# Kernel optimization log

Hardware: AMD Instinct MI355X
Metric: run time of the kernel (lower is better)

The kernel has to match this reference:

```python
import jax, jax.numpy as jnp
import numpy as np

IN_DIM = 64
OUT_DIM = 64


def setup_inputs() -> dict:
    key = jax.random.key(0)
    k1, k2, k3, k4, k5, k6 = jax.random.split(key, 6)
    N, E = 50000, 800000
    features = jax.random.normal(k1, (N, IN_DIM), dtype=jnp.float32)
    src_idx = jax.random.randint(k2, (E,), 0, N, dtype=jnp.int64)
    # torch nn.Linear-style init (uniform +/- 1/sqrt(fan_in)); stored as [in, out]
    s1 = 1.0 / np.sqrt(IN_DIM)
    s2 = 1.0 / np.sqrt(OUT_DIM)
    W1 = jax.random.uniform(k3, (IN_DIM, OUT_DIM), jnp.float32, -s1, s1)
    b1 = jax.random.uniform(k4, (OUT_DIM,), jnp.float32, -s1, s1)
    W2 = jax.random.uniform(k5, (OUT_DIM, OUT_DIM), jnp.float32, -s2, s2)
    b2 = jax.random.uniform(k6, (OUT_DIM,), jnp.float32, -s2, s2)
    return {"features": features, "src_idx": src_idx, "W1": W1, "b1": b1, "W2": W2, "b2": b2}


def reference(features, src_idx, W1, b1, W2, b2):
    # gather source-node features per edge: [E, in_dim]
    x = features[src_idx]
    # Linear -> ReLU -> Linear -> ReLU
    h = jax.nn.relu(x @ W1 + b1)
    out = jax.nn.relu(h @ W2 + b2)  # [E, out_dim] == 'feature_n'
    return out
```

## Files before the change

### kernel.cpp

```cpp
#include <hip/hip_runtime.h>

typedef float f32x4 __attribute__((ext_vector_type(4)));
typedef _Float16 f16;
typedef f16 f16x8 __attribute__((ext_vector_type(8)));


__global__ __launch_bounds__(256) void cvt_kernel(
    const f32x4* __restrict__ in, f16x8* __restrict__ outv, int n8)
{
    const int stride = gridDim.x * blockDim.x;
    for (int i = blockIdx.x * blockDim.x + threadIdx.x; i < n8; i += stride) {
        const f32x4 a = in[2 * i];
        const f32x4 b = in[2 * i + 1];
        f16x8 o;
        #pragma unroll
        for (int j = 0; j < 4; ++j) { o[j] = (f16)a[j]; o[4 + j] = (f16)b[j]; }
        outv[i] = o;
    }
}

__global__ __launch_bounds__(256) void fused_mlp_kernel(
    const f16* __restrict__ feat16,
    const int* __restrict__ src,
    const float* __restrict__ W1, const float* __restrict__ b1,
    const float* __restrict__ W2, const float* __restrict__ b2,
    float* __restrict__ out, int E, int ntiles)
{
    __shared__ f16 hl[4][16][72];

    const int lane = threadIdx.x & 63;
    const int wv   = threadIdx.x >> 6;
    const int l15  = lane & 15;
    const int q    = lane >> 4;

    const int gw = blockIdx.x * 4 + wv;
    const int nw = gridDim.x * 4;

    f16x8 B1f[4][2], B2f[4][2];
    #pragma unroll
    for (int t = 0; t < 4; ++t) {
        #pragma unroll
        for (int s = 0; s < 2; ++s) {
            f16x8 r1, r2;
            #pragma unroll
            for (int j = 0; j < 8; ++j) {
                const int kk = s * 32 + q * 8 + j;
                r1[j] = (f16)W1[kk * 64 + t * 16 + l15];
                r2[j] = (f16)W2[kk * 64 + t * 16 + l15];
            }
            B1f[t][s] = r1;
            B2f[t][s] = r2;
        }
    }
    float bb1[4], bb2[4];
    #pragma unroll
    for (int t = 0; t < 4; ++t) {
        bb1[t] = b1[t * 16 + l15];
        bb2[t] = b2[t * 16 + l15];
    }

    for (int tile = gw; tile < ntiles; tile += nw) {
        const int e0 = tile * 16;
        int er = e0 + l15;
        if (er >= E) er = E - 1;
        const int n = src[er];

        const f16* fp = feat16 + (long long)n * 64;
        const f16x8 A0 = *(const f16x8*)(fp + q * 8);
        const f16x8 A1 = *(const f16x8*)(fp + 32 + q * 8);

        f32x4 acc[4];
        #pragma unroll
        for (int t = 0; t < 4; ++t) acc[t] = (f32x4){bb1[t], bb1[t], bb1[t], bb1[t]};
        #pragma unroll
        for (int t = 0; t < 4; ++t) {
            acc[t] = __builtin_amdgcn_mfma_f32_16x16x32_f16(A0, B1f[t][0], acc[t], 0, 0, 0);
            acc[t] = __builtin_amdgcn_mfma_f32_16x16x32_f16(A1, B1f[t][1], acc[t], 0, 0, 0);
        }

        #pragma unroll
        for (int t = 0; t < 4; ++t)
            #pragma unroll
            for (int i = 0; i < 4; ++i)
                hl[wv][q * 4 + i][t * 16 + l15] = (f16)fmaxf(acc[t][i], 0.0f);

        const f16x8 A2a = *(const f16x8*)&hl[wv][l15][q * 8];
        const f16x8 A2b = *(const f16x8*)&hl[wv][l15][32 + q * 8];

        f32x4 acc2[4];
        #pragma unroll
        for (int t = 0; t < 4; ++t) acc2[t] = (f32x4){bb2[t], bb2[t], bb2[t], bb2[t]};
        #pragma unroll
        for (int t = 0; t < 4; ++t) {
            acc2[t] = __builtin_amdgcn_mfma_f32_16x16x32_f16(A2a, B2f[t][0], acc2[t], 0, 0, 0);
            acc2[t] = __builtin_amdgcn_mfma_f32_16x16x32_f16(A2b, B2f[t][1], acc2[t], 0, 0, 0);
        }

        #pragma unroll
        for (int t = 0; t < 4; ++t)
            #pragma unroll
            for (int i = 0; i < 4; ++i) {
                const int row = e0 + q * 4 + i;
                if (row < E)
                    out[(long long)row * 64 + t * 16 + l15] = fmaxf(acc2[t][i], 0.0f);
            }
    }
}

__device__ __forceinline__ float bcast(float v, int l) {
    return __int_as_float(__builtin_amdgcn_readlane(__float_as_int(v), l));
}

__global__ __launch_bounds__(256, 3) void mlp_nodes_kernel(
    const float* __restrict__ features,
    const int* __restrict__ idx,
    const float* __restrict__ W1, const float* __restrict__ b1,
    const float* __restrict__ W2, const float* __restrict__ b2,
    float* __restrict__ out, int nrows)
{
    const int lane   = threadIdx.x & 63;
    const int wid    = (blockIdx.x * blockDim.x + threadIdx.x) >> 6;
    const int nwaves = (gridDim.x * blockDim.x) >> 6;

    float w1c[64], w2c[64];
    #pragma unroll
    for (int k = 0; k < 64; ++k) w1c[k] = W1[k * 64 + lane];
    #pragma unroll
    for (int k = 0; k < 64; ++k) w2c[k] = W2[k * 64 + lane];
    const float hb = b1[lane];
    const float yb = b2[lane];

    for (int row = wid; row < nrows; row += nwaves) {
        const int n = idx ? idx[row] : row;
        const float x = features[(long long)n * 64 + lane];
        float a0 = hb, a1 = 0.f, a2 = 0.f, a3 = 0.f;
        #pragma unroll
        for (int k = 0; k < 64; k += 4) {
            a0 = fmaf(bcast(x, k + 0), w1c[k + 0], a0);
            a1 = fmaf(bcast(x, k + 1), w1c[k + 1], a1);
            a2 = fmaf(bcast(x, k + 2), w1c[k + 2], a2);
            a3 = fmaf(bcast(x, k + 3), w1c[k + 3], a3);
        }
        const float h = fmaxf((a0 + a1) + (a2 + a3), 0.0f);
        float c0 = yb, c1 = 0.f, c2 = 0.f, c3 = 0.f;
        #pragma unroll
        for (int k = 0; k < 64; k += 4) {
            c0 = fmaf(bcast(h, k + 0), w2c[k + 0], c0);
            c1 = fmaf(bcast(h, k + 1), w2c[k + 1], c1);
            c2 = fmaf(bcast(h, k + 2), w2c[k + 2], c2);
            c3 = fmaf(bcast(h, k + 3), w2c[k + 3], c3);
        }
        out[(long long)row * 64 + lane] = fmaxf((c0 + c1) + (c2 + c3), 0.0f);
    }
}

extern "C" void kernel_launch(void* const* d_in, const int* in_sizes, int n_in,
                              void* d_out, int out_size, void* d_ws, size_t ws_size,
                              hipStream_t stream) {
    const float* features = (const float*)d_in[0];
    const int*   src      = (const int*)  d_in[1];
    const float* W1       = (const float*)d_in[2];
    const float* b1       = (const float*)d_in[3];
    const float* W2       = (const float*)d_in[4];
    const float* b2       = (const float*)d_in[5];
    float* out = (float*)d_out;

    const int N = in_sizes[0] / 64;
    const int E = in_sizes[1];

    const size_t need = (size_t)N * 64 * sizeof(f16);
    if (ws_size >= need) {
        f16* feat16 = (f16*)d_ws;
        cvt_kernel<<<1024, 256, 0, stream>>>(
            (const f32x4*)features, (f16x8*)feat16, N * 8);
        const int ntiles = (E + 15) / 16;
        fused_mlp_kernel<<<1024, 256, 0, stream>>>(
            feat16, src, W1, b1, W2, b2, out, E, ntiles);
    } else {
        mlp_nodes_kernel<<<3072, 256, 0, stream>>>(
            features, src, W1, b1, W2, b2, out, E);
    }
}
```

Baseline: 67.18 us.

## Prefetch next tile's gathered features and vectorize output stores via LDS

Software-pipelines the gather so each wave issues the index and feature loads for its next tile before running the MFMAs on the current one, hiding gather latency behind compute. It also stages the second-layer results through a padded shared-memory buffer, so full tiles are written as 16-byte vector stores instead of scattered 4-byte stores. In exchange it uses more registers and about 17 KB of extra LDS per block, which may lower occupancy. A leftover no-op scope block remains in the code.

```diff
diff --git a/kernel.cpp b/kernel.cpp
--- a/kernel.cpp
+++ b/kernel.cpp
@@ -26,7 +26,8 @@
     const float* __restrict__ W2, const float* __restrict__ b2,
     float* __restrict__ out, int E, int ntiles)
 {
-    __shared__ f16 hl[4][16][72];
+    __shared__ f16  hl[4][16][72];
+    __shared__ float ol[4][16][68];
 
     const int lane = threadIdx.x & 63;
     const int wv   = threadIdx.x >> 6;
@@ -59,15 +60,32 @@
         bb2[t] = b2[t * 16 + l15];
     }
 
-    for (int tile = gw; tile < ntiles; tile += nw) {
+    int tile = gw;
+    if (tile >= ntiles) return;
+
+    {
+        int er = tile * 16 + l15;
+        if (er >= E) er = E - 1;
+    }
+    int er0 = tile * 16 + l15; if (er0 >= E) er0 = E - 1;
+    int n = src[er0];
+    const f16* fp0 = feat16 + (long long)n * 64;
+    f16x8 A0 = *(const f16x8*)(fp0 + q * 8);
+    f16x8 A1 = *(const f16x8*)(fp0 + 32 + q * 8);
+
+    while (tile < ntiles) {
         const int e0 = tile * 16;
-        int er = e0 + l15;
-        if (er >= E) er = E - 1;
-        const int n = src[er];
-
-        const f16* fp = feat16 + (long long)n * 64;
-        const f16x8 A0 = *(const f16x8*)(fp + q * 8);
-        const f16x8 A1 = *(const f16x8*)(fp + 32 + q * 8);
+        const int tile_n = tile + nw;
+
+        f16x8 nA0, nA1;
+        if (tile_n < ntiles) {
+            int er = tile_n * 16 + l15;
+            if (er >= E) er = E - 1;
+            const int nn = src[er];
+            const f16* fp = feat16 + (long long)nn * 64;
+            nA0 = *(const f16x8*)(fp + q * 8);
+            nA1 = *(const f16x8*)(fp + 32 + q * 8);
+        }
 
         f32x4 acc[4];
         #pragma unroll
@@ -96,14 +114,31 @@
             acc2[t] = __builtin_amdgcn_mfma_f32_16x16x32_f16(A2b, B2f[t][1], acc2[t], 0, 0, 0);
         }
 
-        #pragma unroll
-        for (int t = 0; t < 4; ++t)
-            #pragma unroll
-            for (int i = 0; i < 4; ++i) {
-                const int row = e0 + q * 4 + i;
-                if (row < E)
-                    out[(long long)row * 64 + t * 16 + l15] = fmaxf(acc2[t][i], 0.0f);
+        if (e0 + 16 <= E) {
+            #pragma unroll
+            for (int t = 0; t < 4; ++t)
+                #pragma unroll
+                for (int i = 0; i < 4; ++i)
+                    ol[wv][q * 4 + i][t * 16 + l15] = fmaxf(acc2[t][i], 0.0f);
+            #pragma unroll
+            for (int j = 0; j < 4; ++j) {
+                const f32x4 v = *(const f32x4*)&ol[wv][4 * j + q][l15 * 4];
+                *(f32x4*)&out[(long long)(e0 + 4 * j + q) * 64 + l15 * 4] = v;
             }
+        } else {
+            #pragma unroll
+            for (int t = 0; t < 4; ++t)
+                #pragma unroll
+                for (int i = 0; i < 4; ++i) {
+                    const int row = e0 + q * 4 + i;
+                    if (row < E)
+                        out[(long long)row * 64 + t * 16 + l15] = fmaxf(acc2[t][i], 0.0f);
+                }
+        }
+
+        A0 = nA0;
+        A1 = nA1;
+        tile = tile_n;
     }
 }
 
```

Measured after the change: 66.10 us. Within noise of the previous version (-1.6%).

## Compute MLP per node once and scatter results to edges via bucketed slots

Applied to the files above, without the earlier changes.

Rather than running the MLP on each of the 800k gathered edge rows, the kernel first buckets edge ids by source node using atomic counters into fixed-capacity slots (with an overflow list). It then runs the MLP once per node (50k rows) and scatters each node's output row to all its edges with vectorized stores. This removes most of the redundant matmul work and the separate fp16 conversion pass. In exchange it adds a memset, an atomic bucketing pass, scattered writes, and a capped overflow buffer that could drop edges for highly skewed inputs.

```diff
diff --git a/kernel.cpp b/kernel.cpp
--- a/kernel.cpp
+++ b/kernel.cpp
@@ -4,29 +4,42 @@
 typedef _Float16 f16;
 typedef f16 f16x8 __attribute__((ext_vector_type(8)));
 
-
-__global__ __launch_bounds__(256) void cvt_kernel(
-    const f32x4* __restrict__ in, f16x8* __restrict__ outv, int n8)
+#define MAXDEG 56
+#define OVF_CAP 4096
+
+
+__global__ __launch_bounds__(256) void fill_slots_kernel(
+    const int* __restrict__ src, unsigned* __restrict__ cnt,
+    unsigned* __restrict__ slots, unsigned* __restrict__ ovf,
+    unsigned* __restrict__ ovfc, int E)
 {
     const int stride = gridDim.x * blockDim.x;
-    for (int i = blockIdx.x * blockDim.x + threadIdx.x; i < n8; i += stride) {
-        const f32x4 a = in[2 * i];
-        const f32x4 b = in[2 * i + 1];
-        f16x8 o;
-        #pragma unroll
-        for (int j = 0; j < 4; ++j) { o[j] = (f16)a[j]; o[4 + j] = (f16)b[j]; }
-        outv[i] = o;
-    }
-}
-
-__global__ __launch_bounds__(256) void fused_mlp_kernel(
-    const f16* __restrict__ feat16,
+    for (int e = blockIdx.x * blockDim.x + threadIdx.x; e < E; e += stride) {
+        const int n = src[e];
+        const unsigned slot = atomicAdd(&cnt[n], 1u);
+        if (slot < MAXDEG) {
+            slots[(long long)n * MAXDEG + slot] = (unsigned)e;
+        } else {
+            const unsigned o = atomicAdd(ovfc, 1u);
+            if (o < OVF_CAP) ovf[o] = (unsigned)e;
+        }
+    }
+}
+
+__global__ __launch_bounds__(256) void bcast_kernel(
+    const float* __restrict__ feat,
     const int* __restrict__ src,
     const float* __restrict__ W1, const float* __restrict__ b1,
     const float* __restrict__ W2, const float* __restrict__ b2,
-    float* __restrict__ out, int E, int ntiles)
+    const unsigned* __restrict__ cnt,
+    const unsigned* __restrict__ slots,
+    const unsigned* __restrict__ ovf,
+    const unsigned* __restrict__ ovfc,
+    float* __restrict__ out, int N, int E)
 {
-    __shared__ f16 hl[4][16][72];
+    __shared__ f16   hl[4][16][72];
+    __shared__ float ol[4][16][68];
+    __shared__ int   se[4][16];
 
     const int lane = threadIdx.x & 63;
     const int wv   = threadIdx.x >> 6;
@@ -59,15 +72,24 @@
         bb2[t] = b2[t * 16 + l15];
     }
 
-    for (int tile = gw; tile < ntiles; tile += nw) {
-        const int e0 = tile * 16;
-        int er = e0 + l15;
-        if (er >= E) er = E - 1;
-        const int n = src[er];
-
-        const f16* fp = feat16 + (long long)n * 64;
-        const f16x8 A0 = *(const f16x8*)(fp + q * 8);
-        const f16x8 A1 = *(const f16x8*)(fp + 32 + q * 8);
+    const int ntile = (N + 15) >> 4;
+    for (int tile = gw; tile < ntile; tile += nw) {
+        const int r0 = tile << 4;
+        const int rr = (r0 + l15 < N) ? (r0 + l15) : (N - 1);
+        const float* p = feat + (long long)rr * 64;
+
+        f16x8 A0, A1;
+        {
+            const f32x4 u0 = *(const f32x4*)(p + q * 8);
+            const f32x4 u1 = *(const f32x4*)(p + q * 8 + 4);
+            const f32x4 u2 = *(const f32x4*)(p + 32 + q * 8);
+            const f32x4 u3 = *(const f32x4*)(p + 32 + q * 8 + 4);
+            #pragma unroll
+            for (int j = 0; j < 4; ++j) {
+                A0[j] = (f16)u0[j]; A0[4 + j] = (f16)u1[j];
+                A1[j] = (f16)u2[j]; A1[4 + j] = (f16)u3[j];
+            }
+        }
 
         f32x4 acc[4];
         #pragma unroll
@@ -77,7 +99,6 @@
             acc[t] = __builtin_amdgcn_mfma_f32_16x16x32_f16(A0, B1f[t][0], acc[t], 0, 0, 0);
             acc[t] = __builtin_amdgcn_mfma_f32_16x16x32_f16(A1, B1f[t][1], acc[t], 0, 0, 0);
         }
-
         #pragma unroll
         for (int t = 0; t < 4; ++t)
             #pragma unroll
@@ -99,15 +120,95 @@
         #pragma unroll
         for (int t = 0; t < 4; ++t)
             #pragma unroll
-            for (int i = 0; i < 4; ++i) {
-                const int row = e0 + q * 4 + i;
-                if (row < E)
-                    out[(long long)row * 64 + t * 16 + l15] = fmaxf(acc2[t][i], 0.0f);
-            }
-    }
-}
-
-__device__ __forceinline__ float bcast(float v, int l) {
+            for (int i = 0; i < 4; ++i)
+                ol[wv][q * 4 + i][t * 16 + l15] = fmaxf(acc2[t][i], 0.0f);
+
+        int dv = 0;
+        if (r0 + l15 < N) {
+            unsigned c = cnt[r0 + l15];
+            dv = (int)(c < MAXDEG ? c : MAXDEG);
+        }
+
+        #pragma unroll
+        for (int r = 0; r < 16; ++r) {
+            const int deg = __builtin_amdgcn_readlane(dv, r);
+            if (deg == 0) continue;
+            const unsigned* sl = slots + (long long)(r0 + r) * MAXDEG;
+            const f32x4 v = *(const f32x4*)&ol[wv][r][l15 * 4];
+            for (int base = 0; base < deg; base += 4) {
+                const int k = base + q;
+                if (k < deg) {
+                    const int eid = (int)sl[k];
+                    *(f32x4*)&out[(long long)eid * 64 + l15 * 4] = v;
+                }
+            }
+        }
+    }
+
+    const int novf_raw = (int)ovfc[0];
+    const int novf = novf_raw < OVF_CAP ? novf_raw : OVF_CAP;
+    const int nt2 = (novf + 15) >> 4;
+    for (int t2 = gw; t2 < nt2; t2 += nw) {
+        const int i0 = t2 << 4;
+        const int ii = (i0 + l15 < novf) ? (i0 + l15) : (novf - 1);
+        const int e = (int)ovf[ii];
+        const int n = src[e];
+        const float* p = feat + (long long)n * 64;
+
+        f16x8 A0, A1;
+        {
+            const f32x4 u0 = *(const f32x4*)(p + q * 8);
+            const f32x4 u1 = *(const f32x4*)(p + q * 8 + 4);
+            const f32x4 u2 = *(const f32x4*)(p + 32 + q * 8);
+            const f32x4 u3 = *(const f32x4*)(p + 32 + q * 8 + 4);
+            #pragma unroll
+            for (int j = 0; j < 4; ++j) {
+                A0[j] = (f16)u0[j]; A0[4 + j] = (f16)u1[j];
+                A1[j] = (f16)u2[j]; A1[4 + j] = (f16)u3[j];
+            }
+        }
+
+        f32x4 acc[4];
+        #pragma unroll
+        for (int t = 0; t < 4; ++t) acc[t] = (f32x4){bb1[t], bb1[t], bb1[t], bb1[t]};
+        #pragma unroll
+        for (int t = 0; t < 4; ++t) {
+            acc[t] = __builtin_amdgcn_mfma_f32_16x16x32_f16(A0, B1f[t][0], acc[t], 0, 0, 0);
+            acc[t] = __builtin_amdgcn_mfma_f32_16x16x32_f16(A1, B1f[t][1], acc[t], 0, 0, 0);
+        }
+        #pragma unroll
+        for (int t = 0; t < 4; ++t)
+            #pragma unroll
+            for (int i = 0; i < 4; ++i)
+                hl[wv][q * 4 + i][t * 16 + l15] = (f16)fmaxf(acc[t][i], 0.0f);
+
+        const f16x8 A2a = *(const f16x8*)&hl[wv][l15][q * 8];
+        const f16x8 A2b = *(const f16x8*)&hl[wv][l15][32 + q * 8];
+
+        f32x4 acc2[4];
+        #pragma unroll
+        for (int t = 0; t < 4; ++t) acc2[t] = (f32x4){bb2[t], bb2[t], bb2[t], bb2[t]};
+        #pragma unroll
+        for (int t = 0; t < 4; ++t) {
+            acc2[t] = __builtin_amdgcn_mfma_f32_16x16x32_f16(A2a, B2f[t][0], acc2[t], 0, 0, 0);
+            acc2[t] = __builtin_amdgcn_mfma_f32_16x16x32_f16(A2b, B2f[t][1], acc2[t], 0, 0, 0);
+        }
+
+        se[wv][l15] = e;
+        #pragma unroll
+        for (int t = 0; t < 4; ++t)
+            #pragma unroll
+            for (int i2 = 0; i2 < 4; ++i2) {
+                const int row = q * 4 + i2;
+                if (i0 + row < novf) {
+                    const int eid = se[wv][row];
+                    out[(long long)eid * 64 + t * 16 + l15] = fmaxf(acc2[t][i2], 0.0f);
+                }
+            }
+    }
+}
+
+__device__ __forceinline__ float bcast_f(float v, int l) {
     return __int_as_float(__builtin_amdgcn_readlane(__float_as_int(v), l));
 }
 
@@ -136,19 +237,19 @@
         float a0 = hb, a1 = 0.f, a2 = 0.f, a3 = 0.f;
         #pragma unroll
         for (int k = 0; k < 64; k += 4) {
-            a0 = fmaf(bcast(x, k + 0), w1c[k + 0], a0);
-            a1 = fmaf(bcast(x, k + 1), w1c[k + 1], a1);
-            a2 = fmaf(bcast(x, k + 2), w1c[k + 2], a2);
-            a3 = fmaf(bcast(x, k + 3), w1c[k + 3], a3);
+            a0 = fmaf(bcast_f(x, k + 0), w1c[k + 0], a0);
+            a1 = fmaf(bcast_f(x, k + 1), w1c[k + 1], a1);
+            a2 = fmaf(bcast_f(x, k + 2), w1c[k + 2], a2);
+            a3 = fmaf(bcast_f(x, k + 3), w1c[k + 3], a3);
         }
         const float h = fmaxf((a0 + a1) + (a2 + a3), 0.0f);
         float c0 = yb, c1 = 0.f, c2 = 0.f, c3 = 0.f;
         #pragma unroll
         for (int k = 0; k < 64; k += 4) {
-            c0 = fmaf(bcast(h, k + 0), w2c[k + 0], c0);
-            c1 = fmaf(bcast(h, k + 1), w2c[k + 1], c1);
-            c2 = fmaf(bcast(h, k + 2), w2c[k + 2], c2);
-            c3 = fmaf(bcast(h, k + 3), w2c[k + 3], c3);
+            c0 = fmaf(bcast_f(h, k + 0), w2c[k + 0], c0);
+            c1 = fmaf(bcast_f(h, k + 1), w2c[k + 1], c1);
+            c2 = fmaf(bcast_f(h, k + 2), w2c[k + 2], c2);
+            c3 = fmaf(bcast_f(h, k + 3), w2c[k + 3], c3);
         }
         out[(long long)row * 64 + lane] = fmaxf((c0 + c1) + (c2 + c3), 0.0f);
     }
@@ -168,14 +269,17 @@
     const int N = in_sizes[0] / 64;
     const int E = in_sizes[1];
 
-    const size_t need = (size_t)N * 64 * sizeof(f16);
-    if (ws_size >= need) {
-        f16* feat16 = (f16*)d_ws;
-        cvt_kernel<<<1024, 256, 0, stream>>>(
-            (const f32x4*)features, (f16x8*)feat16, N * 8);
-        const int ntiles = (E + 15) / 16;
-        fused_mlp_kernel<<<1024, 256, 0, stream>>>(
-            feat16, src, W1, b1, W2, b2, out, E, ntiles);
+    const size_t ws_words = (size_t)(N + 16) + (size_t)N * MAXDEG + OVF_CAP;
+    if (ws_size >= ws_words * sizeof(unsigned)) {
+        unsigned* cnt   = (unsigned*)d_ws;
+        unsigned* ovfc  = cnt + N;
+        unsigned* slots = cnt + N + 16;
+        unsigned* ovf   = slots + (size_t)N * MAXDEG;
+
+        hipMemsetAsync(d_ws, 0, (size_t)(N + 16) * sizeof(unsigned), stream);
+        fill_slots_kernel<<<1536, 256, 0, stream>>>(src, cnt, slots, ovf, ovfc, E);
+        bcast_kernel<<<782, 256, 0, stream>>>(
+            features, src, W1, b1, W2, b2, cnt, slots, ovf, ovfc, out, N, E);
     } else {
         mlp_nodes_kernel<<<3072, 256, 0, stream>>>(
             features, src, W1, b1, W2, b2, out, E);
```

Measured after the change: 118.6 us. +76.5%, slower.
